# Optimization experiments

Measured on AMD Instinct MI355X. Metric: run time of the kernel, lower is better.

The kernel has to match this reference:

```python
import jax, jax.numpy as jnp
import numpy as np

B, S, HID = 2, 2048, 1024
NH, NKV, HD = 8, 2, 256
G = NH // NKV              # kv groups (repeat factor)
ROT = 128                  # rotary_dim (partial RoPE)
EPS = 1e-6
SCALE = HD ** -0.5


def _rmsnorm(x, w, eps=EPS):
    # Qwen35RMSNorm: fp32 norm, (1 + weight) scale
    xf = x.astype(jnp.float32)
    n = xf * jax.lax.rsqrt(jnp.mean(xf * xf, axis=-1, keepdims=True) + eps)
    return (n * (1.0 + w.astype(jnp.float32))).astype(x.dtype)


def _rotate_half(x):
    h = x.shape[-1] // 2
    return jnp.concatenate([-x[..., h:], x[..., :h]], axis=-1)


def setup_inputs() -> dict:
    key = jax.random.key(0)
    ks = jax.random.split(key, 8)
    hidden_states = jax.random.normal(ks[0], (B, S, HID), jnp.float32)
    # realistic RoPE tables: freqs of dim ROT/2, duplicated -> ROT
    pos = jnp.arange(S, dtype=jnp.float32)
    inv_freq = 1.0 / (10000.0 ** (jnp.arange(0, ROT, 2, dtype=jnp.float32) / ROT))
    f = pos[:, None] * inv_freq[None, :]            # [S, ROT/2]
    emb = jnp.concatenate([f, f], axis=-1)          # [S, ROT]
    cos = jnp.broadcast_to(jnp.cos(emb)[None], (B, S, ROT)).astype(jnp.float32)
    sin = jnp.broadcast_to(jnp.sin(emb)[None], (B, S, ROT)).astype(jnp.float32)
    std = 0.02
    Wq = jax.random.normal(ks[1], (HID, NH * HD * 2), jnp.float32) * std
    Wk = jax.random.normal(ks[2], (HID, NKV * HD), jnp.float32) * std
    Wv = jax.random.normal(ks[3], (HID, NKV * HD), jnp.float32) * std
    Wo = jax.random.normal(ks[4], (NH * HD, HID), jnp.float32) * std
    q_norm_w = jax.random.normal(ks[5], (HD,), jnp.float32) * std
    k_norm_w = jax.random.normal(ks[6], (HD,), jnp.float32) * std
    return dict(hidden_states=hidden_states, cos=cos, sin=sin,
                Wq=Wq, Wk=Wk, Wv=Wv, Wo=Wo,
                q_norm_w=q_norm_w, k_norm_w=k_norm_w)


def reference(hidden_states, cos, sin, Wq, Wk, Wv, Wo, q_norm_w, k_norm_w):
    b, s, _ = hidden_states.shape
    # projections (Linear with weight stored [in, out])
    qg = (hidden_states @ Wq).reshape(b, s, NH, HD * 2)
    q, gate = qg[..., :HD], qg[..., HD:]            # [b,s,NH,HD] each
    gate = gate.reshape(b, s, NH * HD)
    q = _rmsnorm(q, q_norm_w)
    k = _rmsnorm((hidden_states @ Wk).reshape(b, s, NKV, HD), k_norm_w)
    v = (hidden_states @ Wv).reshape(b, s, NKV, HD)
    # partial RoPE on first ROT dims; cos/sin broadcast over heads
    c = cos[:, :, None, :]
    sn = sin[:, :, None, :]
    q_rot = q[..., :ROT] * c + _rotate_half(q[..., :ROT]) * sn
    k_rot = k[..., :ROT] * c + _rotate_half(k[..., :ROT]) * sn
    q = jnp.concatenate([q_rot, q[..., ROT:]], axis=-1)
    k = jnp.concatenate([k_rot, k[..., ROT:]], axis=-1)
    # GQA without materializing repeated KV: group q heads per kv head
    qr = q.reshape(b, s, NKV, G, HD)                # repeat_interleave layout
    scores = jnp.einsum('bqkgd,bskd->bkgqs', qr, k) * SCALE   # [b,NKV,G,S,S]
    mask = jnp.tril(jnp.ones((s, s), dtype=bool))
    scores = jnp.where(mask, scores, jnp.float32(-jnp.inf))
    probs = jax.nn.softmax(scores, axis=-1)
    out = jnp.einsum('bkgqs,bskd->bqkgd', probs, v).reshape(b, s, NH * HD)
    out = out * jax.nn.sigmoid(gate)
    return out @ Wo
```

## Files before the change

kernel.cpp:

```cpp
#include <hip/hip_runtime.h>
#include <cstdint>
#include <cstddef>

#define B_ 2
#define S_ 2048
#define HID_ 1024
#define NH_ 8
#define NKV_ 2
#define HD_ 256
#define ROT_ 128
#define TOK_ (B_ * S_)
#define SCALE_ 0.0625f

typedef __attribute__((ext_vector_type(8))) short s16x8;
typedef __attribute__((ext_vector_type(4))) float f32x4;

__device__ __forceinline__ float bf2f(short u) {
  unsigned t = ((unsigned)(unsigned short)u) << 16;
  float f;
  __builtin_memcpy(&f, &t, 4);
  return f;
}
__device__ __forceinline__ short f2bf(float f) {
  unsigned u;
  __builtin_memcpy(&u, &f, 4);
  u += 0x7fffu + ((u >> 16) & 1);
  return (short)(u >> 16);
}

__device__ __forceinline__ void gl16(const void* g, void* l) {
  __builtin_amdgcn_global_load_lds((const __attribute__((address_space(1))) int*)g,
                                   (__attribute__((address_space(3))) int*)l, 16, 0, 0);
}

__global__ __launch_bounds__(256) void k_cast(const float* __restrict__ in,
                                              short* __restrict__ out, int n) {
  int i = blockIdx.x * 256 + threadIdx.x;
  if (i < n) out[i] = f2bf(in[i]);
}

__global__ __launch_bounds__(256) void k_wtrans(const float* __restrict__ in,
                                                short* __restrict__ out, int R, int C) {
  __shared__ short tile[32][33];
  int tx = threadIdx.x & 31, ty = threadIdx.x >> 5;
  int r0 = blockIdx.y * 32, c0 = blockIdx.x * 32;
#pragma unroll
  for (int p = 0; p < 4; ++p)
    tile[ty + p * 8][tx] = f2bf(in[(size_t)(r0 + ty + p * 8) * C + c0 + tx]);
  __syncthreads();
#pragma unroll
  for (int p = 0; p < 4; ++p)
    out[(size_t)(c0 + ty + p * 8) * R + r0 + tx] = tile[tx][ty + p * 8];
}

__global__ __launch_bounds__(256) void k_vtrans(const short* __restrict__ kvp,
                                                short* __restrict__ Vtg) {
  __shared__ short tile[32][33];
  int bh = blockIdx.z;
  int b = bh >> 1, kvh = bh & 1;
  int s0 = blockIdx.x * 32, d0 = blockIdx.y * 32;
  int tx = threadIdx.x & 31, ty = threadIdx.x >> 5;
#pragma unroll
  for (int p = 0; p < 4; ++p) {
    int sr = ty + p * 8;
    tile[sr][tx] = kvp[(size_t)(b * S_ + s0 + sr) * 1024 + 512 + kvh * 256 + d0 + tx];
  }
  __syncthreads();
#pragma unroll
  for (int p = 0; p < 4; ++p) {
    int dr = ty + p * 8;
    Vtg[((size_t)bh * 256 + d0 + dr) * 2048 + s0 + tx] = tile[tx][dr];
  }
}

template <int OUT_BF16>
__global__ __launch_bounds__(256, 2) void k_gemm_bt(const short* __restrict__ A,
                                                    const short* __restrict__ Bt,
                                                    void* __restrict__ Cv, int M, int N,
                                                    int K) {
  extern __shared__ char smem[];
  const int tid = threadIdx.x;
  const int bm = blockIdx.y * 128, bn = blockIdx.x * 128;
  const int w = tid >> 6, lane = tid & 63, lo = lane & 15, hi = lane >> 4;
  const int wr = (w >> 1) * 64, wc = (w & 1) * 64;
  f32x4 acc[4][4] = {};

  auto stage = [&](int k0, int nb) {
#pragma unroll
    for (int rnd = 0; rnd < 4; ++rnd) {
      int i = rnd * 256 + tid;
      int row = i >> 3, c = i & 7;
      int src_col = (c ^ (row & 7)) * 8;
      gl16(&A[(size_t)(bm + row) * K + k0 + src_col], smem + (size_t)nb * 16384 + (size_t)i * 16);
      gl16(&Bt[(size_t)(bn + row) * K + k0 + src_col],
           smem + 32768 + (size_t)nb * 16384 + (size_t)i * 16);
    }
  };

  stage(0, 0);
  __syncthreads();
  int nb = 0;
  for (int k0 = 0; k0 < K; k0 += 64) {
    if (k0 + 64 < K) stage(k0 + 64, nb ^ 1);
    const short* As = (const short*)(smem + (size_t)nb * 16384);
    const short* Bs = (const short*)(smem + 32768 + (size_t)nb * 16384);
    s16x8 af[2][4], bfr[2][4];
#pragma unroll
    for (int kk = 0; kk < 2; ++kk) {
#pragma unroll
      for (int m = 0; m < 4; ++m) {
        int row = wr + m * 16 + lo;
        af[kk][m] = *(const s16x8*)&As[row * 64 + (((kk * 4 + hi) ^ (row & 7)) * 8)];
      }
#pragma unroll
      for (int n = 0; n < 4; ++n) {
        int row = wc + n * 16 + lo;
        bfr[kk][n] = *(const s16x8*)&Bs[row * 64 + (((kk * 4 + hi) ^ (row & 7)) * 8)];
      }
    }
#pragma unroll
    for (int kk = 0; kk < 2; ++kk)
#pragma unroll
      for (int m = 0; m < 4; ++m)
#pragma unroll
        for (int n = 0; n < 4; ++n)
          acc[m][n] =
              __builtin_amdgcn_mfma_f32_16x16x32_bf16(af[kk][m], bfr[kk][n], acc[m][n], 0, 0, 0);
    __syncthreads();
    nb ^= 1;
  }
#pragma unroll
  for (int m = 0; m < 4; ++m)
#pragma unroll
    for (int n = 0; n < 4; ++n)
#pragma unroll
      for (int r = 0; r < 4; ++r) {
        int row = bm + wr + m * 16 + hi * 4 + r;
        int col = bn + wc + n * 16 + lo;
        if (OUT_BF16)
          ((short*)Cv)[(size_t)row * N + col] = f2bf(acc[m][n][r]);
        else
          ((float*)Cv)[(size_t)row * N + col] = acc[m][n][r];
      }
}

template <int OUT_BF16>
__global__ __launch_bounds__(512, 1) void k_gemm256(const short* __restrict__ A,
                                                    const short* __restrict__ Bt,
                                                    void* __restrict__ Cv, int M, int N,
                                                    int K) {
  extern __shared__ char smem[];
  const int tid = threadIdx.x;
  const int bm = blockIdx.y * 256, bn = blockIdx.x * 256;
  const int w = tid >> 6, lane = tid & 63, lo = lane & 15, hi = lane >> 4;
  const int wr = (w >> 2) * 128, wc = (w & 3) * 64;
  f32x4 acc[8][4] = {};

  auto stage = [&](int k0, int nb) {
#pragma unroll
    for (int rnd = 0; rnd < 4; ++rnd) {
      int i = rnd * 512 + tid;
      int row = i >> 3, c = i & 7;
      int src_col = (c ^ (row & 7)) * 8;
      gl16(&A[(size_t)(bm + row) * K + k0 + src_col], smem + (size_t)nb * 32768 + (size_t)i * 16);
      gl16(&Bt[(size_t)(bn + row) * K + k0 + src_col],
           smem + 65536 + (size_t)nb * 32768 + (size_t)i * 16);
    }
  };

  stage(0, 0);
  __syncthreads();
  int nb = 0;
  for (int k0 = 0; k0 < K; k0 += 64) {
    if (k0 + 64 < K) stage(k0 + 64, nb ^ 1);
    const short* As = (const short*)(smem + (size_t)nb * 32768);
    const short* Bs = (const short*)(smem + 65536 + (size_t)nb * 32768);
#pragma unroll
    for (int kk = 0; kk < 2; ++kk) {
      s16x8 bfr[4];
#pragma unroll
      for (int n = 0; n < 4; ++n) {
        int row = wc + n * 16 + lo;
        bfr[n] = *(const s16x8*)&Bs[row * 64 + (((kk * 4 + hi) ^ (row & 7)) * 8)];
      }
#pragma unroll
      for (int g = 0; g < 2; ++g) {
        s16x8 af[4];
#pragma unroll
        for (int u = 0; u < 4; ++u) {
          int row = wr + (g * 4 + u) * 16 + lo;
          af[u] = *(const s16x8*)&As[row * 64 + (((kk * 4 + hi) ^ (row & 7)) * 8)];
        }
#pragma unroll
        for (int u = 0; u < 4; ++u)
#pragma unroll
          for (int n = 0; n < 4; ++n)
            acc[g * 4 + u][n] =
                __builtin_amdgcn_mfma_f32_16x16x32_bf16(af[u], bfr[n], acc[g * 4 + u][n], 0, 0, 0);
      }
    }
    __syncthreads();
    nb ^= 1;
  }
#pragma unroll
  for (int m = 0; m < 8; ++m)
#pragma unroll
    for (int n = 0; n < 4; ++n)
#pragma unroll
      for (int r = 0; r < 4; ++r) {
        int row = bm + wr + m * 16 + hi * 4 + r;
        int col = bn + wc + n * 16 + lo;
        if (OUT_BF16)
          ((short*)Cv)[(size_t)row * N + col] = f2bf(acc[m][n][r]);
        else
          ((float*)Cv)[(size_t)row * N + col] = acc[m][n][r];
      }
}

template <int NHEAD, int IN_ROW, int IN_HS>
__global__ __launch_bounds__(256) void k_norm_rope(const short* __restrict__ xin,
                                                   const float* __restrict__ wn,
                                                   const float* __restrict__ cosb,
                                                   const float* __restrict__ sinb,
                                                   short* __restrict__ xout) {
  int blk = blockIdx.x;
  int h = blk % NHEAD;
  int ts = blk / NHEAD;
  int d = threadIdx.x;
  float x = bf2f(xin[(size_t)ts * IN_ROW + h * IN_HS + d]);
  float ss = x * x;
#pragma unroll
  for (int m = 32; m >= 1; m >>= 1) ss += __shfl_xor(ss, m);
  __shared__ float sred[4];
  __shared__ float sn[256];
  int wid = d >> 6;
  if ((d & 63) == 0) sred[wid] = ss;
  __syncthreads();
  float tot = sred[0] + sred[1] + sred[2] + sred[3];
  float nv = x * rsqrtf(tot * (1.0f / 256.0f) + 1e-6f) * (1.0f + wn[d]);
  sn[d] = nv;
  __syncthreads();
  float o;
  if (d < 128) {
    float c = cosb[(size_t)ts * 128 + d];
    float s = sinb[(size_t)ts * 128 + d];
    o = (d < 64) ? (nv * c - sn[d + 64] * s) : (nv * c + sn[d - 64] * s);
  } else {
    o = nv;
  }
  xout[(size_t)blk * 256 + d] = f2bf(o);
}

#define ATTN_LDS 131072
__global__ __launch_bounds__(512, 1) void k_attn(const short* __restrict__ qb,
                                                 const short* __restrict__ kb,
                                                 const short* __restrict__ Vtg,
                                                 const short* __restrict__ qg,
                                                 short* __restrict__ og) {
  extern __shared__ char smem[];
  short* KbufS = (short*)smem;
  short* VbufS = (short*)(smem + 65536);

  const int raw = blockIdx.x;
  const int xcd = raw & 7, slot = raw >> 3;
  const int p = xcd >> 1, side = xcd & 1;
  const int id = side * 32 + slot;
  const int hgi = id & 3, qt = id >> 2;
  const int b = p >> 1, kvh = p & 1, h = kvh * 4 + hgi;
  const int q0 = qt * 128;
  const int tid = threadIdx.x;
  const int w = tid >> 6, lane = tid & 63, lo = lane & 15, hi = lane >> 4;
  const int swz = lo & 7;

  const short* kbase = kb + ((size_t)(b * S_) * NKV_ + kvh) * HD_;
  const short* vbase = Vtg + (size_t)(b * 2 + kvh) * 256 * 2048;

  auto stage = [&](int kv0, int nb) {
#pragma unroll
    for (int rnd = 0; rnd < 4; ++rnd) {
      int i = rnd * 512 + tid;
      {
        int row = i >> 5, c = i & 31;
        const short* src = kbase + (size_t)(kv0 + row) * 512 + ((c ^ (row & 7)) * 8);
        gl16(src, smem + (size_t)nb * 32768 + (size_t)i * 16);
      }
      {
        int row = i >> 3, c = i & 7;
        const short* src = vbase + (size_t)row * 2048 + kv0 + ((c ^ (row & 7)) * 8);
        gl16(src, smem + 65536 + (size_t)nb * 32768 + (size_t)i * 16);
      }
    }
  };

  s16x8 qf[8];
  {
    size_t base = ((size_t)((b * S_ + q0 + w * 16 + lo) * NH_) + h) * HD_;
#pragma unroll
    for (int t = 0; t < 8; ++t) qf[t] = *(const s16x8*)&qb[base + t * 32 + hi * 8];
  }
  f32x4 acc[16];
#pragma unroll
  for (int t = 0; t < 16; ++t) acc[t] = (f32x4){0.f, 0.f, 0.f, 0.f};
  float m_run = -1e30f, l_run = 0.f;
  const int qrow = q0 + w * 16 + lo;

  stage(0, 0);
  __syncthreads();

  const int ntiles = 2 * qt + 2;
  int n = 0;
#pragma unroll 1
  for (int it = 0; it < ntiles; ++it) {
    const int kv0 = it * 64;
    if (it + 1 < ntiles) stage(kv0 + 64, n ^ 1);

    const short* Kb = KbufS + n * 16384;
    const short* Vb = VbufS + n * 16384;

    f32x4 sacc[4] = {};
#pragma unroll
    for (int nt = 0; nt < 4; ++nt) {
      s16x8 kf[8];
#pragma unroll
      for (int t = 0; t < 8; ++t)
        kf[t] = *(const s16x8*)&Kb[(nt * 16 + lo) * 256 + (((t * 4 + hi) ^ swz) * 8)];
#pragma unroll
      for (int t = 0; t < 8; ++t)
        sacc[nt] = __builtin_amdgcn_mfma_f32_16x16x32_bf16(kf[t], qf[t], sacc[nt], 0, 0, 0);
    }

    float pv[4][4];
    float mx = -1e30f;
#pragma unroll
    for (int nt = 0; nt < 4; ++nt)
#pragma unroll
      for (int r = 0; r < 4; ++r) {
        int kv = kv0 + nt * 16 + hi * 4 + r;
        float s = sacc[nt][r] * SCALE_;
        if (kv > qrow) s = -1e30f;
        pv[nt][r] = s;
        mx = fmaxf(mx, s);
      }
    mx = fmaxf(mx, __shfl_xor(mx, 16));
    mx = fmaxf(mx, __shfl_xor(mx, 32));
    if (!__all(mx <= m_run + 8.f)) {
      float mnew = fmaxf(m_run, mx);
      float fs = __expf(m_run - mnew);
      m_run = mnew;
      l_run *= fs;
      float f0 = __shfl(fs, 4 * hi + 0);
      float f1 = __shfl(fs, 4 * hi + 1);
      float f2 = __shfl(fs, 4 * hi + 2);
      float f3 = __shfl(fs, 4 * hi + 3);
#pragma unroll
      for (int t = 0; t < 16; ++t) {
        acc[t][0] *= f0;
        acc[t][1] *= f1;
        acc[t][2] *= f2;
        acc[t][3] *= f3;
      }
    }
    float rs = 0.f;
#pragma unroll
    for (int nt = 0; nt < 4; ++nt)
#pragma unroll
      for (int r = 0; r < 4; ++r) {
        pv[nt][r] = __expf(pv[nt][r] - m_run);
        rs += pv[nt][r];
      }
    rs += __shfl_xor(rs, 16);
    rs += __shfl_xor(rs, 32);
    l_run += rs;

    int pk0[4], pk1[4];
#pragma unroll
    for (int nt = 0; nt < 4; ++nt) {
      asm("v_cvt_pk_bf16_f32 %0, %1, %2" : "=v"(pk0[nt]) : "v"(pv[nt][0]), "v"(pv[nt][1]));
      asm("v_cvt_pk_bf16_f32 %0, %1, %2" : "=v"(pk1[nt]) : "v"(pv[nt][2]), "v"(pv[nt][3]));
    }

#pragma unroll
    for (int ks = 0; ks < 2; ++ks) {
      int pw[4];
#pragma unroll
      for (int dw = 0; dw < 4; ++dw) {
        int srcl = (2 * (hi & 1) + (dw >> 1)) * 16 + lo;
        int vA = __shfl((dw & 1) ? pk1[2 * ks] : pk0[2 * ks], srcl);
        int vB = __shfl((dw & 1) ? pk1[2 * ks + 1] : pk0[2 * ks + 1], srcl);
        pw[dw] = (hi & 2) ? vB : vA;
      }
      s16x8 pa;
      __builtin_memcpy(&pa, pw, 16);
#pragma unroll
      for (int g = 0; g < 2; ++g) {
        s16x8 vf[8];
#pragma unroll
        for (int u = 0; u < 8; ++u) {
          int t = g * 8 + u;
          vf[u] = *(const s16x8*)&Vb[(t * 16 + lo) * 64 + (((ks * 4 + hi) ^ swz) * 8)];
        }
#pragma unroll
        for (int u = 0; u < 8; ++u) {
          int t = g * 8 + u;
          acc[t] = __builtin_amdgcn_mfma_f32_16x16x32_bf16(pa, vf[u], acc[t], 0, 0, 0);
        }
      }
    }
    __syncthreads();
    n ^= 1;
  }

  float linv[4];
#pragma unroll
  for (int r = 0; r < 4; ++r) linv[r] = 1.0f / __shfl(l_run, 4 * hi + r);
#pragma unroll
  for (int t = 0; t < 16; ++t)
#pragma unroll
    for (int r = 0; r < 4; ++r) {
      int row = q0 + w * 16 + hi * 4 + r;
      int hd = t * 16 + lo;
      float o = acc[t][r] * linv[r];
      float g = bf2f(qg[(size_t)(b * S_ + row) * 4096 + h * 512 + 256 + hd]);
      float sg = 1.0f / (1.0f + __expf(-g));
      og[(size_t)(b * S_ + row) * 2048 + h * 256 + hd] = f2bf(o * sg);
    }
}

extern "C" void kernel_launch(void* const* d_in, const int* in_sizes, int n_in, void* d_out,
                              int out_size, void* d_ws, size_t ws_size, hipStream_t stream) {
  const float* hidden = (const float*)d_in[0];
  const float* cosb = (const float*)d_in[1];
  const float* sinb = (const float*)d_in[2];
  const float* Wq = (const float*)d_in[3];
  const float* Wk = (const float*)d_in[4];
  const float* Wv = (const float*)d_in[5];
  const float* Wo = (const float*)d_in[6];
  const float* qw = (const float*)d_in[7];
  const float* kw = (const float*)d_in[8];
  float* out = (float*)d_out;

  char* ws = (char*)d_ws;
  size_t off = 0;
  auto alloc = [&](size_t bytes) {
    void* p = ws + off;
    off += (bytes + 255) & ~(size_t)255;
    return p;
  };
  short* hb = (short*)alloc((size_t)TOK_ * HID_ * 2);
  short* WqT = (short*)alloc((size_t)4096 * 1024 * 2);
  short* kvT = (short*)alloc((size_t)1024 * 1024 * 2);
  short* WoT = (short*)alloc((size_t)1024 * 2048 * 2);
  short* qg = (short*)alloc((size_t)TOK_ * 4096 * 2);
  short* kvp = (short*)alloc((size_t)TOK_ * 1024 * 2);
  short* qb = (short*)alloc((size_t)TOK_ * 2048 * 2);
  short* kb = (short*)alloc((size_t)TOK_ * 512 * 2);
  short* og = (short*)alloc((size_t)TOK_ * 2048 * 2);
  short* Vtg = WqT;
  (void)ws_size;
  (void)in_sizes;
  (void)n_in;
  (void)out_size;

  hipFuncSetAttribute((const void*)k_attn, hipFuncAttributeMaxDynamicSharedMemorySize,
                      ATTN_LDS);
  hipFuncSetAttribute((const void*)k_gemm256<1>, hipFuncAttributeMaxDynamicSharedMemorySize,
                      131072);
  hipFuncSetAttribute((const void*)k_gemm_bt<1>, hipFuncAttributeMaxDynamicSharedMemorySize,
                      65536);
  hipFuncSetAttribute((const void*)k_gemm_bt<0>, hipFuncAttributeMaxDynamicSharedMemorySize,
                      65536);

  k_cast<<<(TOK_ * HID_ + 255) / 256, 256, 0, stream>>>(hidden, hb, TOK_ * HID_);
  k_wtrans<<<dim3(4096 / 32, 1024 / 32), 256, 0, stream>>>(Wq, WqT, 1024, 4096);
  k_wtrans<<<dim3(512 / 32, 1024 / 32), 256, 0, stream>>>(Wk, kvT, 1024, 512);
  k_wtrans<<<dim3(512 / 32, 1024 / 32), 256, 0, stream>>>(Wv, kvT + 512 * 1024, 1024, 512);
  k_wtrans<<<dim3(1024 / 32, 2048 / 32), 256, 0, stream>>>(Wo, WoT, 2048, 1024);

  k_gemm256<1><<<dim3(16, 16), 512, 131072, stream>>>(hb, WqT, qg, 4096, 4096, 1024);
  k_gemm_bt<1><<<dim3(8, 32), 256, 65536, stream>>>(hb, kvT, kvp, 4096, 1024, 1024);

  k_norm_rope<NH_, 4096, 512><<<TOK_ * NH_, 256, 0, stream>>>(qg, qw, cosb, sinb, qb);
  k_norm_rope<NKV_, 1024, 256><<<TOK_ * NKV_, 256, 0, stream>>>(kvp, kw, cosb, sinb, kb);
  k_vtrans<<<dim3(64, 8, 4), 256, 0, stream>>>(kvp, Vtg);

  k_attn<<<256, 512, ATTN_LDS, stream>>>(qb, kb, Vtg, qg, og);

  k_gemm_bt<0><<<dim3(8, 32), 256, 65536, stream>>>(og, WoT, out, 4096, 1024, 2048);
}
```

Measured before the change: 232.9 us.

## Use 32x32x16 MFMA in attention with split-KV warps and LDS merge

Moves the attention kernel from 16x16x32 to 32x32x16 bf16 MFMA tiles. Each wave now owns 32 query rows and half of each 64-key tile, so the 8 waves form a 4x2 grid over query groups and key halves. Two partial softmax states per query row are merged at the end through LDS, which needs a slightly larger shared-memory allocation. P is repacked with v_permlane32_swap instead of multiple shuffles. The intent is fewer MFMA issues and fewer K/V LDS reads per FLOP, at the cost of an extra end-of-kernel reduction and higher register pressure from 16-wide accumulators.

Result: slower. 326.7 us (+40.3%).

```diff
diff --git a/kernel.cpp b/kernel.cpp
--- a/kernel.cpp
+++ b/kernel.cpp
@@ -14,6 +14,7 @@
 
 typedef __attribute__((ext_vector_type(8))) short s16x8;
 typedef __attribute__((ext_vector_type(4))) float f32x4;
+typedef __attribute__((ext_vector_type(16))) float f32x16;
 
 __device__ __forceinline__ float bf2f(short u) {
   unsigned t = ((unsigned)(unsigned short)u) << 16;
@@ -251,15 +252,17 @@
   xout[(size_t)blk * 256 + d] = f2bf(o);
 }
 
-#define ATTN_LDS 131072
+#define ATTN_LDS 135168
 __global__ __launch_bounds__(512, 1) void k_attn(const short* __restrict__ qb,
                                                  const short* __restrict__ kb,
                                                  const short* __restrict__ Vtg,
-                                                 const short* __restrict__ qg,
+                                                 const short* __restrict__ qgate,
                                                  short* __restrict__ og) {
   extern __shared__ char smem[];
   short* KbufS = (short*)smem;
   short* VbufS = (short*)(smem + 65536);
+  float* Obuf = (float*)smem;
+  float* mlbuf = (float*)(smem + 133120);
 
   const int raw = blockIdx.x;
   const int xcd = raw & 7, slot = raw >> 3;
@@ -269,8 +272,9 @@
   const int b = p >> 1, kvh = p & 1, h = kvh * 4 + hgi;
   const int q0 = qt * 128;
   const int tid = threadIdx.x;
-  const int w = tid >> 6, lane = tid & 63, lo = lane & 15, hi = lane >> 4;
-  const int swz = lo & 7;
+  const int w = tid >> 6, lane = tid & 63;
+  const int l31 = lane & 31, hi32 = lane >> 5;
+  const int qg_ = w & 3, kh = w >> 2;
 
   const short* kbase = kb + ((size_t)(b * S_) * NKV_ + kvh) * HD_;
   const short* vbase = Vtg + (size_t)(b * 2 + kvh) * 256 * 2048;
@@ -292,17 +296,19 @@
     }
   };
 
-  s16x8 qf[8];
+  s16x8 qf[16];
   {
-    size_t base = ((size_t)((b * S_ + q0 + w * 16 + lo) * NH_) + h) * HD_;
-#pragma unroll
-    for (int t = 0; t < 8; ++t) qf[t] = *(const s16x8*)&qb[base + t * 32 + hi * 8];
-  }
-  f32x4 acc[16];
-#pragma unroll
-  for (int t = 0; t < 16; ++t) acc[t] = (f32x4){0.f, 0.f, 0.f, 0.f};
+    size_t base = ((size_t)((b * S_ + q0 + qg_ * 32 + l31) * NH_) + h) * HD_;
+#pragma unroll
+    for (int c = 0; c < 16; ++c) qf[c] = *(const s16x8*)&qb[base + c * 16 + hi32 * 8];
+  }
+  f32x16 acc[8];
+#pragma unroll
+  for (int d0 = 0; d0 < 8; ++d0)
+#pragma unroll
+    for (int r = 0; r < 16; ++r) acc[d0][r] = 0.f;
   float m_run = -1e30f, l_run = 0.f;
-  const int qrow = q0 + w * 16 + lo;
+  const int qrow_g = q0 + qg_ * 32 + l31;
 
   stage(0, 0);
   __syncthreads();
@@ -317,113 +323,123 @@
     const short* Kb = KbufS + n * 16384;
     const short* Vb = VbufS + n * 16384;
 
-    f32x4 sacc[4] = {};
-#pragma unroll
-    for (int nt = 0; nt < 4; ++nt) {
-      s16x8 kf[8];
-#pragma unroll
-      for (int t = 0; t < 8; ++t)
-        kf[t] = *(const s16x8*)&Kb[(nt * 16 + lo) * 256 + (((t * 4 + hi) ^ swz) * 8)];
-#pragma unroll
-      for (int t = 0; t < 8; ++t)
-        sacc[nt] = __builtin_amdgcn_mfma_f32_16x16x32_bf16(kf[t], qf[t], sacc[nt], 0, 0, 0);
-    }
-
-    float pv[4][4];
+    f32x16 sacc;
+#pragma unroll
+    for (int r = 0; r < 16; ++r) sacc[r] = 0.f;
+    {
+      const int krow = kh * 32 + l31;
+      const int ksw = krow & 7;
+#pragma unroll
+      for (int c = 0; c < 16; ++c) {
+        s16x8 kf = *(const s16x8*)&Kb[krow * 256 + (((c * 2 + hi32) ^ ksw) * 8)];
+        sacc = __builtin_amdgcn_mfma_f32_32x32x16_bf16(kf, qf[c], sacc, 0, 0, 0);
+      }
+    }
+
+    float pl[16];
     float mx = -1e30f;
 #pragma unroll
-    for (int nt = 0; nt < 4; ++nt)
-#pragma unroll
-      for (int r = 0; r < 4; ++r) {
-        int kv = kv0 + nt * 16 + hi * 4 + r;
-        float s = sacc[nt][r] * SCALE_;
-        if (kv > qrow) s = -1e30f;
-        pv[nt][r] = s;
-        mx = fmaxf(mx, s);
-      }
-    mx = fmaxf(mx, __shfl_xor(mx, 16));
+    for (int r = 0; r < 16; ++r) {
+      int kvg = kv0 + kh * 32 + (r & 3) + 8 * (r >> 2) + 4 * hi32;
+      float v = sacc[r] * SCALE_;
+      if (kvg > qrow_g) v = -1e30f;
+      pl[r] = v;
+      mx = fmaxf(mx, v);
+    }
     mx = fmaxf(mx, __shfl_xor(mx, 32));
     if (!__all(mx <= m_run + 8.f)) {
       float mnew = fmaxf(m_run, mx);
       float fs = __expf(m_run - mnew);
       m_run = mnew;
       l_run *= fs;
-      float f0 = __shfl(fs, 4 * hi + 0);
-      float f1 = __shfl(fs, 4 * hi + 1);
-      float f2 = __shfl(fs, 4 * hi + 2);
-      float f3 = __shfl(fs, 4 * hi + 3);
-#pragma unroll
-      for (int t = 0; t < 16; ++t) {
-        acc[t][0] *= f0;
-        acc[t][1] *= f1;
-        acc[t][2] *= f2;
-        acc[t][3] *= f3;
+#pragma unroll
+      for (int r = 0; r < 16; ++r) {
+        float fr = __shfl(fs, (r & 3) + 8 * (r >> 2) + 4 * hi32);
+#pragma unroll
+        for (int d0 = 0; d0 < 8; ++d0) acc[d0][r] *= fr;
       }
     }
     float rs = 0.f;
 #pragma unroll
-    for (int nt = 0; nt < 4; ++nt)
-#pragma unroll
-      for (int r = 0; r < 4; ++r) {
-        pv[nt][r] = __expf(pv[nt][r] - m_run);
-        rs += pv[nt][r];
-      }
-    rs += __shfl_xor(rs, 16);
+    for (int r = 0; r < 16; ++r) {
+      pl[r] = __expf(pl[r] - m_run);
+      rs += pl[r];
+    }
     rs += __shfl_xor(rs, 32);
     l_run += rs;
 
-    int pk0[4], pk1[4];
-#pragma unroll
-    for (int nt = 0; nt < 4; ++nt) {
-      asm("v_cvt_pk_bf16_f32 %0, %1, %2" : "=v"(pk0[nt]) : "v"(pv[nt][0]), "v"(pv[nt][1]));
-      asm("v_cvt_pk_bf16_f32 %0, %1, %2" : "=v"(pk1[nt]) : "v"(pv[nt][2]), "v"(pv[nt][3]));
+    int pk[4][2];
+#pragma unroll
+    for (int bq = 0; bq < 4; ++bq) {
+      asm("v_cvt_pk_bf16_f32 %0, %1, %2" : "=v"(pk[bq][0]) : "v"(pl[4 * bq]), "v"(pl[4 * bq + 1]));
+      asm("v_cvt_pk_bf16_f32 %0, %1, %2"
+          : "=v"(pk[bq][1])
+          : "v"(pl[4 * bq + 2]), "v"(pl[4 * bq + 3]));
     }
 
 #pragma unroll
     for (int ks = 0; ks < 2; ++ks) {
-      int pw[4];
-#pragma unroll
-      for (int dw = 0; dw < 4; ++dw) {
-        int srcl = (2 * (hi & 1) + (dw >> 1)) * 16 + lo;
-        int vA = __shfl((dw & 1) ? pk1[2 * ks] : pk0[2 * ks], srcl);
-        int vB = __shfl((dw & 1) ? pk1[2 * ks + 1] : pk0[2 * ks + 1], srcl);
-        pw[dw] = (hi & 2) ? vB : vA;
-      }
+      int e00 = pk[2 * ks][0], e10 = pk[2 * ks + 1][0];
+      int e01 = pk[2 * ks][1], e11 = pk[2 * ks + 1][1];
+      asm("v_permlane32_swap_b32 %0, %1" : "+v"(e00), "+v"(e10));
+      asm("v_permlane32_swap_b32 %0, %1" : "+v"(e01), "+v"(e11));
+      int pw[4] = {e00, e01, e10, e11};
       s16x8 pa;
       __builtin_memcpy(&pa, pw, 16);
 #pragma unroll
-      for (int g = 0; g < 2; ++g) {
-        s16x8 vf[8];
-#pragma unroll
-        for (int u = 0; u < 8; ++u) {
-          int t = g * 8 + u;
-          vf[u] = *(const s16x8*)&Vb[(t * 16 + lo) * 64 + (((ks * 4 + hi) ^ swz) * 8)];
-        }
-#pragma unroll
-        for (int u = 0; u < 8; ++u) {
-          int t = g * 8 + u;
-          acc[t] = __builtin_amdgcn_mfma_f32_16x16x32_bf16(pa, vf[u], acc[t], 0, 0, 0);
-        }
+      for (int d0 = 0; d0 < 8; ++d0) {
+        int vrow = d0 * 32 + l31;
+        s16x8 vf =
+            *(const s16x8*)&Vb[vrow * 64 + (((kh * 4 + ks * 2 + hi32) ^ (vrow & 7)) * 8)];
+        acc[d0] = __builtin_amdgcn_mfma_f32_32x32x16_bf16(pa, vf, acc[d0], 0, 0, 0);
       }
     }
     __syncthreads();
     n ^= 1;
   }
 
-  float linv[4];
-#pragma unroll
-  for (int r = 0; r < 4; ++r) linv[r] = 1.0f / __shfl(l_run, 4 * hi + r);
-#pragma unroll
-  for (int t = 0; t < 16; ++t)
-#pragma unroll
-    for (int r = 0; r < 4; ++r) {
-      int row = q0 + w * 16 + hi * 4 + r;
-      int hd = t * 16 + lo;
-      float o = acc[t][r] * linv[r];
-      float g = bf2f(qg[(size_t)(b * S_ + row) * 4096 + h * 512 + 256 + hd]);
-      float sg = 1.0f / (1.0f + __expf(-g));
-      og[(size_t)(b * S_ + row) * 2048 + h * 256 + hd] = f2bf(o * sg);
-    }
+  if (hi32 == 0) {
+    mlbuf[(kh * 4 + qg_) * 32 + l31] = m_run;
+    mlbuf[256 + (kh * 4 + qg_) * 32 + l31] = l_run;
+  }
+  __syncthreads();
+  float mo = mlbuf[((1 - kh) * 4 + qg_) * 32 + l31];
+  float lo_ = mlbuf[256 + ((1 - kh) * 4 + qg_) * 32 + l31];
+  float mm = fmaxf(m_run, mo);
+  float fs_ = __expf(m_run - mm);
+  float fo_ = __expf(mo - mm);
+  float lt = l_run * fs_ + lo_ * fo_;
+  float fsr[16], linv[16];
+#pragma unroll
+  for (int r = 0; r < 16; ++r) {
+    int qsrc = (r & 3) + 8 * (r >> 2) + 4 * hi32;
+    fsr[r] = __shfl(fs_, qsrc);
+    linv[r] = 1.0f / __shfl(lt, qsrc);
+  }
+  if (kh == 1) {
+#pragma unroll
+    for (int d0 = 0; d0 < 8; ++d0)
+#pragma unroll
+      for (int r = 0; r < 16; ++r) {
+        int ql = qg_ * 32 + (r & 3) + 8 * (r >> 2) + 4 * hi32;
+        Obuf[ql * 260 + d0 * 32 + l31] = acc[d0][r] * fsr[r];
+      }
+  }
+  __syncthreads();
+  if (kh == 0) {
+#pragma unroll
+    for (int d0 = 0; d0 < 8; ++d0)
+#pragma unroll
+      for (int r = 0; r < 16; ++r) {
+        int qloc = (r & 3) + 8 * (r >> 2) + 4 * hi32;
+        int row = q0 + qg_ * 32 + qloc;
+        int hd = d0 * 32 + l31;
+        float o = (acc[d0][r] * fsr[r] + Obuf[(qg_ * 32 + qloc) * 260 + hd]) * linv[r];
+        float g = bf2f(qgate[(size_t)(b * S_ + row) * 4096 + h * 512 + 256 + hd]);
+        float sg = 1.0f / (1.0f + __expf(-g));
+        og[(size_t)(b * S_ + row) * 2048 + h * 256 + hd] = f2bf(o * sg);
+      }
+  }
 }
 
 extern "C" void kernel_launch(void* const* d_in, const int* in_sizes, int n_in, void* d_out,
```

## Triple-buffer k_gemm256 with BK=32 tiles and vmcnt-based single barrier

Applied to the files above, without the earlier changes.

Restructures the Q/gate projection GEMM mainloop from a double-buffered BK=64 pipeline to a three-stage ring of BK=32 tiles. Global loads run two stages ahead, and each iteration ends with one explicit s_waitcnt vmcnt(4) plus an s_barrier. The aim is to hide global-load latency better and replace the implicit full waitcnt of __syncthreads with finer control. In exchange, LDS drops to 96 KB, but there are twice as many barrier iterations with half the MFMA work between them. It also relies on the hand-written waitcnt counts matching the number of loads per stage.

Result: no change. 236.0 us (+1.4%).

```diff
diff --git a/kernel.cpp b/kernel.cpp
--- a/kernel.cpp
+++ b/kernel.cpp
@@ -156,52 +156,71 @@
   const int wr = (w >> 2) * 128, wc = (w & 3) * 64;
   f32x4 acc[8][4] = {};
 
-  auto stage = [&](int k0, int nb) {
-#pragma unroll
-    for (int rnd = 0; rnd < 4; ++rnd) {
+  auto stage = [&](int t, int j) {
+    const int k0 = t * 32;
+#pragma unroll
+    for (int rnd = 0; rnd < 2; ++rnd) {
       int i = rnd * 512 + tid;
-      int row = i >> 3, c = i & 7;
-      int src_col = (c ^ (row & 7)) * 8;
-      gl16(&A[(size_t)(bm + row) * K + k0 + src_col], smem + (size_t)nb * 32768 + (size_t)i * 16);
-      gl16(&Bt[(size_t)(bn + row) * K + k0 + src_col],
-           smem + 65536 + (size_t)nb * 32768 + (size_t)i * 16);
+      int row = i >> 2, c = i & 3;
+      int sc = (c ^ (row & 3)) * 8;
+      gl16(&A[(size_t)(bm + row) * K + k0 + sc], smem + (size_t)j * 16384 + (size_t)i * 16);
+      gl16(&Bt[(size_t)(bn + row) * K + k0 + sc],
+           smem + 49152 + (size_t)j * 16384 + (size_t)i * 16);
     }
   };
-
+  auto compute = [&](int j) {
+    const short* As = (const short*)(smem + (size_t)j * 16384);
+    const short* Bs = (const short*)(smem + 49152 + (size_t)j * 16384);
+    s16x8 bfr[4];
+#pragma unroll
+    for (int n = 0; n < 4; ++n) {
+      int row = wc + n * 16 + lo;
+      bfr[n] = *(const s16x8*)&Bs[row * 32 + ((hi ^ (row & 3)) * 8)];
+    }
+#pragma unroll
+    for (int g = 0; g < 2; ++g) {
+      s16x8 af[4];
+#pragma unroll
+      for (int u = 0; u < 4; ++u) {
+        int row = wr + (g * 4 + u) * 16 + lo;
+        af[u] = *(const s16x8*)&As[row * 32 + ((hi ^ (row & 3)) * 8)];
+      }
+#pragma unroll
+      for (int u = 0; u < 4; ++u)
+#pragma unroll
+        for (int n = 0; n < 4; ++n)
+          acc[g * 4 + u][n] =
+              __builtin_amdgcn_mfma_f32_16x16x32_bf16(af[u], bfr[n], acc[g * 4 + u][n], 0, 0, 0);
+    }
+  };
+
+  const int nt = K >> 5;
   stage(0, 0);
-  __syncthreads();
-  int nb = 0;
-  for (int k0 = 0; k0 < K; k0 += 64) {
-    if (k0 + 64 < K) stage(k0 + 64, nb ^ 1);
-    const short* As = (const short*)(smem + (size_t)nb * 32768);
-    const short* Bs = (const short*)(smem + 65536 + (size_t)nb * 32768);
-#pragma unroll
-    for (int kk = 0; kk < 2; ++kk) {
-      s16x8 bfr[4];
-#pragma unroll
-      for (int n = 0; n < 4; ++n) {
-        int row = wc + n * 16 + lo;
-        bfr[n] = *(const s16x8*)&Bs[row * 64 + (((kk * 4 + hi) ^ (row & 7)) * 8)];
-      }
-#pragma unroll
-      for (int g = 0; g < 2; ++g) {
-        s16x8 af[4];
-#pragma unroll
-        for (int u = 0; u < 4; ++u) {
-          int row = wr + (g * 4 + u) * 16 + lo;
-          af[u] = *(const s16x8*)&As[row * 64 + (((kk * 4 + hi) ^ (row & 7)) * 8)];
-        }
-#pragma unroll
-        for (int u = 0; u < 4; ++u)
-#pragma unroll
-          for (int n = 0; n < 4; ++n)
-            acc[g * 4 + u][n] =
-                __builtin_amdgcn_mfma_f32_16x16x32_bf16(af[u], bfr[n], acc[g * 4 + u][n], 0, 0, 0);
-      }
-    }
-    __syncthreads();
-    nb ^= 1;
-  }
+  stage(1, 1);
+  asm volatile("s_waitcnt vmcnt(4)" ::: "memory");
+  __builtin_amdgcn_sched_barrier(0);
+  __builtin_amdgcn_s_barrier();
+  __builtin_amdgcn_sched_barrier(0);
+  int jc = 0, js = 2;
+#pragma unroll 1
+  for (int t = 0; t < nt - 2; ++t) {
+    stage(t + 2, js);
+    compute(jc);
+    asm volatile("s_waitcnt lgkmcnt(0) vmcnt(4)" ::: "memory");
+    __builtin_amdgcn_sched_barrier(0);
+    __builtin_amdgcn_s_barrier();
+    __builtin_amdgcn_sched_barrier(0);
+    jc = (jc == 2) ? 0 : jc + 1;
+    js = (js == 2) ? 0 : js + 1;
+  }
+  compute(jc);
+  asm volatile("s_waitcnt lgkmcnt(0) vmcnt(0)" ::: "memory");
+  __builtin_amdgcn_sched_barrier(0);
+  __builtin_amdgcn_s_barrier();
+  __builtin_amdgcn_sched_barrier(0);
+  jc = (jc == 2) ? 0 : jc + 1;
+  compute(jc);
+
 #pragma unroll
   for (int m = 0; m < 8; ++m)
 #pragma unroll
@@ -464,7 +483,7 @@
   hipFuncSetAttribute((const void*)k_attn, hipFuncAttributeMaxDynamicSharedMemorySize,
                       ATTN_LDS);
   hipFuncSetAttribute((const void*)k_gemm256<1>, hipFuncAttributeMaxDynamicSharedMemorySize,
-                      131072);
+                      98304);
   hipFuncSetAttribute((const void*)k_gemm_bt<1>, hipFuncAttributeMaxDynamicSharedMemorySize,
                       65536);
   hipFuncSetAttribute((const void*)k_gemm_bt<0>, hipFuncAttributeMaxDynamicSharedMemorySize,
@@ -476,7 +495,7 @@
   k_wtrans<<<dim3(512 / 32, 1024 / 32), 256, 0, stream>>>(Wv, kvT + 512 * 1024, 1024, 512);
   k_wtrans<<<dim3(1024 / 32, 2048 / 32), 256, 0, stream>>>(Wo, WoT, 2048, 1024);
 
-  k_gemm256<1><<<dim3(16, 16), 512, 131072, stream>>>(hb, WqT, qg, 4096, 4096, 1024);
+  k_gemm256<1><<<dim3(16, 16), 512, 98304, stream>>>(hb, WqT, qg, 4096, 4096, 1024);
   k_gemm_bt<1><<<dim3(8, 32), 256, 65536, stream>>>(hb, kvT, kvp, 4096, 1024, 1024);
 
   k_norm_rope<NH_, 4096, 512><<<TOK_ * NH_, 256, 0, stream>>>(qg, qw, cosb, sinb, qb);
```

## Balance causal attention work by splitting KV range and merging partials

Applied to the files above, without the earlier changes.

Each attention block now processes two halves of KV work: the first part of query tile j and the second part of query tile 15-j, so every block does a similar number of KV tiles instead of the triangular imbalance across blocks. The partial outputs, row max and row sum are written to workspace, and a new merge kernel combines the two partials with log-sum-exp weights and applies the sigmoid gate. This costs extra global traffic for the bf16 partials, an extra kernel launch, and some bf16 rounding of the intermediate outputs.

Result: faster. 207.9 us, median of 2 (-10.7%).

```diff
diff --git a/kernel.cpp b/kernel.cpp
--- a/kernel.cpp
+++ b/kernel.cpp
@@ -255,8 +255,9 @@
 __global__ __launch_bounds__(512, 1) void k_attn(const short* __restrict__ qb,
                                                  const short* __restrict__ kb,
                                                  const short* __restrict__ Vtg,
-                                                 const short* __restrict__ qg,
-                                                 short* __restrict__ og) {
+                                                 short* __restrict__ Po,
+                                                 float* __restrict__ Pm,
+                                                 float* __restrict__ Pl) {
   extern __shared__ char smem[];
   short* KbufS = (short*)smem;
   short* VbufS = (short*)(smem + 65536);
@@ -265,9 +266,8 @@
   const int xcd = raw & 7, slot = raw >> 3;
   const int p = xcd >> 1, side = xcd & 1;
   const int id = side * 32 + slot;
-  const int hgi = id & 3, qt = id >> 2;
+  const int hgi = id & 3, j = id >> 2;
   const int b = p >> 1, kvh = p & 1, h = kvh * 4 + hgi;
-  const int q0 = qt * 128;
   const int tid = threadIdx.x;
   const int w = tid >> 6, lane = tid & 63, lo = lane & 15, hi = lane >> 4;
   const int swz = lo & 7;
@@ -292,138 +292,178 @@
     }
   };
 
-  s16x8 qf[8];
-  {
-    size_t base = ((size_t)((b * S_ + q0 + w * 16 + lo) * NH_) + h) * HD_;
-#pragma unroll
-    for (int t = 0; t < 8; ++t) qf[t] = *(const s16x8*)&qb[base + t * 32 + hi * 8];
-  }
-  f32x4 acc[16];
-#pragma unroll
-  for (int t = 0; t < 16; ++t) acc[t] = (f32x4){0.f, 0.f, 0.f, 0.f};
-  float m_run = -1e30f, l_run = 0.f;
-  const int qrow = q0 + w * 16 + lo;
-
-  stage(0, 0);
-  __syncthreads();
-
-  const int ntiles = 2 * qt + 2;
-  int n = 0;
 #pragma unroll 1
-  for (int it = 0; it < ntiles; ++it) {
-    const int kv0 = it * 64;
-    if (it + 1 < ntiles) stage(kv0 + 64, n ^ 1);
-
-    const short* Kb = KbufS + n * 16384;
-    const short* Vb = VbufS + n * 16384;
-
-    f32x4 sacc[4] = {};
-#pragma unroll
-    for (int nt = 0; nt < 4; ++nt) {
-      s16x8 kf[8];
-#pragma unroll
-      for (int t = 0; t < 8; ++t)
-        kf[t] = *(const s16x8*)&Kb[(nt * 16 + lo) * 256 + (((t * 4 + hi) ^ swz) * 8)];
-#pragma unroll
-      for (int t = 0; t < 8; ++t)
-        sacc[nt] = __builtin_amdgcn_mfma_f32_16x16x32_bf16(kf[t], qf[t], sacc[nt], 0, 0, 0);
-    }
-
-    float pv[4][4];
-    float mx = -1e30f;
-#pragma unroll
-    for (int nt = 0; nt < 4; ++nt)
-#pragma unroll
-      for (int r = 0; r < 4; ++r) {
-        int kv = kv0 + nt * 16 + hi * 4 + r;
-        float s = sacc[nt][r] * SCALE_;
-        if (kv > qrow) s = -1e30f;
-        pv[nt][r] = s;
-        mx = fmaxf(mx, s);
-      }
-    mx = fmaxf(mx, __shfl_xor(mx, 16));
-    mx = fmaxf(mx, __shfl_xor(mx, 32));
-    if (!__all(mx <= m_run + 8.f)) {
-      float mnew = fmaxf(m_run, mx);
-      float fs = __expf(m_run - mnew);
-      m_run = mnew;
-      l_run *= fs;
-      float f0 = __shfl(fs, 4 * hi + 0);
-      float f1 = __shfl(fs, 4 * hi + 1);
-      float f2 = __shfl(fs, 4 * hi + 2);
-      float f3 = __shfl(fs, 4 * hi + 3);
-#pragma unroll
-      for (int t = 0; t < 16; ++t) {
-        acc[t][0] *= f0;
-        acc[t][1] *= f1;
-        acc[t][2] *= f2;
-        acc[t][3] *= f3;
-      }
-    }
-    float rs = 0.f;
-#pragma unroll
-    for (int nt = 0; nt < 4; ++nt)
-#pragma unroll
-      for (int r = 0; r < 4; ++r) {
-        pv[nt][r] = __expf(pv[nt][r] - m_run);
-        rs += pv[nt][r];
-      }
-    rs += __shfl_xor(rs, 16);
-    rs += __shfl_xor(rs, 32);
-    l_run += rs;
-
-    int pk0[4], pk1[4];
-#pragma unroll
-    for (int nt = 0; nt < 4; ++nt) {
-      asm("v_cvt_pk_bf16_f32 %0, %1, %2" : "=v"(pk0[nt]) : "v"(pv[nt][0]), "v"(pv[nt][1]));
-      asm("v_cvt_pk_bf16_f32 %0, %1, %2" : "=v"(pk1[nt]) : "v"(pv[nt][2]), "v"(pv[nt][3]));
-    }
-
-#pragma unroll
-    for (int ks = 0; ks < 2; ++ks) {
-      int pw[4];
-#pragma unroll
-      for (int dw = 0; dw < 4; ++dw) {
-        int srcl = (2 * (hi & 1) + (dw >> 1)) * 16 + lo;
-        int vA = __shfl((dw & 1) ? pk1[2 * ks] : pk0[2 * ks], srcl);
-        int vB = __shfl((dw & 1) ? pk1[2 * ks + 1] : pk0[2 * ks + 1], srcl);
-        pw[dw] = (hi & 2) ? vB : vA;
-      }
-      s16x8 pa;
-      __builtin_memcpy(&pa, pw, 16);
-#pragma unroll
-      for (int g = 0; g < 2; ++g) {
-        s16x8 vf[8];
-#pragma unroll
-        for (int u = 0; u < 8; ++u) {
-          int t = g * 8 + u;
-          vf[u] = *(const s16x8*)&Vb[(t * 16 + lo) * 64 + (((ks * 4 + hi) ^ swz) * 8)];
+  for (int part = 0; part < 2; ++part) {
+    const int qt = part ? (15 - j) : j;
+    const int q0 = qt * 128;
+    const int t_begin = part ? (qt + 1) : 0;
+    const int t_end = part ? (2 * qt + 2) : (qt + 1);
+
+    s16x8 qf[8];
+    {
+      size_t base = ((size_t)((b * S_ + q0 + w * 16 + lo) * NH_) + h) * HD_;
+#pragma unroll
+      for (int t = 0; t < 8; ++t) qf[t] = *(const s16x8*)&qb[base + t * 32 + hi * 8];
+    }
+    f32x4 acc[16];
+#pragma unroll
+    for (int t = 0; t < 16; ++t) acc[t] = (f32x4){0.f, 0.f, 0.f, 0.f};
+    float m_run = -1e30f, l_run = 0.f;
+    const int qrow = q0 + w * 16 + lo;
+
+    stage(t_begin * 64, 0);
+    __syncthreads();
+
+    int n = 0;
+#pragma unroll 1
+    for (int it = t_begin; it < t_end; ++it) {
+      const int kv0 = it * 64;
+      if (it + 1 < t_end) stage(kv0 + 64, n ^ 1);
+
+      const short* Kb = KbufS + n * 16384;
+      const short* Vb = VbufS + n * 16384;
+
+      f32x4 sacc[4] = {};
+#pragma unroll
+      for (int nt = 0; nt < 4; ++nt) {
+        s16x8 kf[8];
+#pragma unroll
+        for (int t = 0; t < 8; ++t)
+          kf[t] = *(const s16x8*)&Kb[(nt * 16 + lo) * 256 + (((t * 4 + hi) ^ swz) * 8)];
+#pragma unroll
+        for (int t = 0; t < 8; ++t)
+          sacc[nt] = __builtin_amdgcn_mfma_f32_16x16x32_bf16(kf[t], qf[t], sacc[nt], 0, 0, 0);
+      }
+
+      float pv[4][4];
+      float mx = -1e30f;
+#pragma unroll
+      for (int nt = 0; nt < 4; ++nt)
+#pragma unroll
+        for (int r = 0; r < 4; ++r) {
+          int kv = kv0 + nt * 16 + hi * 4 + r;
+          float s = sacc[nt][r] * SCALE_;
+          if (kv > qrow) s = -1e30f;
+          pv[nt][r] = s;
+          mx = fmaxf(mx, s);
         }
-#pragma unroll
-        for (int u = 0; u < 8; ++u) {
-          int t = g * 8 + u;
-          acc[t] = __builtin_amdgcn_mfma_f32_16x16x32_bf16(pa, vf[u], acc[t], 0, 0, 0);
+      mx = fmaxf(mx, __shfl_xor(mx, 16));
+      mx = fmaxf(mx, __shfl_xor(mx, 32));
+      if (!__all(mx <= m_run + 8.f)) {
+        float mnew = fmaxf(m_run, mx);
+        float fs = __expf(m_run - mnew);
+        m_run = mnew;
+        l_run *= fs;
+        float f0 = __shfl(fs, 4 * hi + 0);
+        float f1 = __shfl(fs, 4 * hi + 1);
+        float f2 = __shfl(fs, 4 * hi + 2);
+        float f3 = __shfl(fs, 4 * hi + 3);
+#pragma unroll
+        for (int t = 0; t < 16; ++t) {
+          acc[t][0] *= f0;
+          acc[t][1] *= f1;
+          acc[t][2] *= f2;
+          acc[t][3] *= f3;
         }
       }
-    }
-    __syncthreads();
-    n ^= 1;
-  }
-
-  float linv[4];
-#pragma unroll
-  for (int r = 0; r < 4; ++r) linv[r] = 1.0f / __shfl(l_run, 4 * hi + r);
-#pragma unroll
-  for (int t = 0; t < 16; ++t)
+      float rs = 0.f;
+#pragma unroll
+      for (int nt = 0; nt < 4; ++nt)
+#pragma unroll
+        for (int r = 0; r < 4; ++r) {
+          pv[nt][r] = __expf(pv[nt][r] - m_run);
+          rs += pv[nt][r];
+        }
+      rs += __shfl_xor(rs, 16);
+      rs += __shfl_xor(rs, 32);
+      l_run += rs;
+
+      int pk0[4], pk1[4];
+#pragma unroll
+      for (int nt = 0; nt < 4; ++nt) {
+        asm("v_cvt_pk_bf16_f32 %0, %1, %2" : "=v"(pk0[nt]) : "v"(pv[nt][0]), "v"(pv[nt][1]));
+        asm("v_cvt_pk_bf16_f32 %0, %1, %2" : "=v"(pk1[nt]) : "v"(pv[nt][2]), "v"(pv[nt][3]));
+      }
+
+#pragma unroll
+      for (int ks = 0; ks < 2; ++ks) {
+        int pw[4];
+#pragma unroll
+        for (int dw = 0; dw < 4; ++dw) {
+          int srcl = (2 * (hi & 1) + (dw >> 1)) * 16 + lo;
+          int vA = __shfl((dw & 1) ? pk1[2 * ks] : pk0[2 * ks], srcl);
+          int vB = __shfl((dw & 1) ? pk1[2 * ks + 1] : pk0[2 * ks + 1], srcl);
+          pw[dw] = (hi & 2) ? vB : vA;
+        }
+        s16x8 pa;
+        __builtin_memcpy(&pa, pw, 16);
+#pragma unroll
+        for (int g = 0; g < 2; ++g) {
+          s16x8 vf[8];
+#pragma unroll
+          for (int u = 0; u < 8; ++u) {
+            int t = g * 8 + u;
+            vf[u] = *(const s16x8*)&Vb[(t * 16 + lo) * 64 + (((ks * 4 + hi) ^ swz) * 8)];
+          }
+#pragma unroll
+          for (int u = 0; u < 8; ++u) {
+            int t = g * 8 + u;
+            acc[t] = __builtin_amdgcn_mfma_f32_16x16x32_bf16(pa, vf[u], acc[t], 0, 0, 0);
+          }
+        }
+      }
+      __syncthreads();
+      n ^= 1;
+    }
+
+    const int tile2 = ((b * 8 + h) * 16 + qt) * 2 + part;
+    float linv[4];
 #pragma unroll
     for (int r = 0; r < 4; ++r) {
-      int row = q0 + w * 16 + hi * 4 + r;
-      int hd = t * 16 + lo;
-      float o = acc[t][r] * linv[r];
-      float g = bf2f(qg[(size_t)(b * S_ + row) * 4096 + h * 512 + 256 + hd]);
-      float sg = 1.0f / (1.0f + __expf(-g));
-      og[(size_t)(b * S_ + row) * 2048 + h * 256 + hd] = f2bf(o * sg);
-    }
+      float lr = __shfl(l_run, 4 * hi + r);
+      linv[r] = lr > 0.f ? 1.0f / lr : 0.f;
+    }
+#pragma unroll
+    for (int t = 0; t < 16; ++t)
+#pragma unroll
+      for (int r = 0; r < 4; ++r)
+        Po[(size_t)tile2 * 32768 + (w * 16 + hi * 4 + r) * 256 + t * 16 + lo] =
+            f2bf(acc[t][r] * linv[r]);
+    if (hi == 0) {
+      Pm[tile2 * 128 + w * 16 + lo] = m_run;
+      Pl[tile2 * 128 + w * 16 + lo] = l_run;
+    }
+  }
+}
+
+__global__ __launch_bounds__(256) void k_merge(const short* __restrict__ Po,
+                                               const float* __restrict__ Pm,
+                                               const float* __restrict__ Pl,
+                                               const short* __restrict__ qg,
+                                               short* __restrict__ og) {
+  const int tile = blockIdx.x >> 4, rc = blockIdx.x & 15;
+  const int b = tile >> 7, h = (tile >> 4) & 7, qt = tile & 15;
+  const int t = threadIdx.x;
+  const int r = t >> 5, rl = rc * 8 + r, c0 = (t & 31) * 8;
+  const int row = qt * 128 + rl;
+  const size_t base = (size_t)tile * 2 * 32768;
+  s16x8 o0 = *(const s16x8*)&Po[base + rl * 256 + c0];
+  s16x8 o1 = *(const s16x8*)&Po[base + 32768 + rl * 256 + c0];
+  float m0 = Pm[tile * 256 + rl], m1 = Pm[tile * 256 + 128 + rl];
+  float l0 = Pl[tile * 256 + rl], l1 = Pl[tile * 256 + 128 + rl];
+  float mm = fmaxf(m0, m1);
+  float w0 = l0 * __expf(m0 - mm), w1 = l1 * __expf(m1 - mm);
+  float inv = 1.0f / (w0 + w1);
+  s16x8 gv = *(const s16x8*)&qg[(size_t)(b * S_ + row) * 4096 + h * 512 + 256 + c0];
+  s16x8 outv;
+#pragma unroll
+  for (int jj = 0; jj < 8; ++jj) {
+    float o = (w0 * bf2f(o0[jj]) + w1 * bf2f(o1[jj])) * inv;
+    float g = bf2f(gv[jj]);
+    float sg = 1.0f / (1.0f + __expf(-g));
+    outv[jj] = f2bf(o * sg);
+  }
+  *(s16x8*)&og[(size_t)(b * S_ + row) * 2048 + h * 256 + c0] = outv;
 }
 
 extern "C" void kernel_launch(void* const* d_in, const int* in_sizes, int n_in, void* d_out,
@@ -455,6 +495,9 @@
   short* qb = (short*)alloc((size_t)TOK_ * 2048 * 2);
   short* kb = (short*)alloc((size_t)TOK_ * 512 * 2);
   short* og = (short*)alloc((size_t)TOK_ * 2048 * 2);
+  short* Po = (short*)alloc((size_t)512 * 32768 * 2);
+  float* Pm = (float*)alloc((size_t)512 * 128 * 4);
+  float* Pl = (float*)alloc((size_t)512 * 128 * 4);
   short* Vtg = WqT;
   (void)ws_size;
   (void)in_sizes;
@@ -483,7 +526,8 @@
   k_norm_rope<NKV_, 1024, 256><<<TOK_ * NKV_, 256, 0, stream>>>(kvp, kw, cosb, sinb, kb);
   k_vtrans<<<dim3(64, 8, 4), 256, 0, stream>>>(kvp, Vtg);
 
-  k_attn<<<256, 512, ATTN_LDS, stream>>>(qb, kb, Vtg, qg, og);
+  k_attn<<<256, 512, ATTN_LDS, stream>>>(qb, kb, Vtg, Po, Pm, Pl);
+  k_merge<<<4096, 256, 0, stream>>>(Po, Pm, Pl, qg, og);
 
   k_gemm_bt<0><<<dim3(8, 32), 256, 65536, stream>>>(og, WoT, out, 4096, 1024, 2048);
 }
```
